# Performance work log

Hardware: AMD Instinct MI355X
Metric: run time of the kernel (lower is better)

## Reference

```python
import jax, jax.numpy as jnp
import numpy as np
import math

V, L, H, D, T_MAX, FF = 50257, 12, 12, 768, 1024, 3072
B, T = 2, 1024
HD = D // H


def layernorm(x, g, b, eps=1e-5):
    m = x.mean(-1, keepdims=True)
    v = ((x - m) ** 2).mean(-1, keepdims=True)
    return (x - m) / jnp.sqrt(v + eps) * g + b


def mgelu(x):
    # note: module uses 0.047715 (not the standard 0.044715)
    return 0.5 * x * (1.0 + jnp.tanh(math.sqrt(2.0 / math.pi) * (x + 0.047715 * x ** 3)))


def setup_inputs() -> dict:
    key = jax.random.key(0)
    ks = jax.random.split(key, 16)
    s = 0.02
    sr = 0.02 * (2 * L) ** -0.5  # residual-projection init per GPT2 paper
    inp = {
        "idx": jax.random.randint(ks[0], (B, T), 0, V),
        "targets": jax.random.randint(ks[1], (B, T), 0, V),
        "wte": jax.random.normal(ks[2], (V, D), jnp.float32) * s,
        "wpe": jax.random.normal(ks[3], (T_MAX, D), jnp.float32) * s,
        "ln1_g": jnp.ones((L, D), jnp.float32),
        "ln1_b": jnp.zeros((L, D), jnp.float32),
        "qkv_w": jax.random.normal(ks[4], (L, D, 3 * D), jnp.float32) * s,
        "qkv_b": jnp.zeros((L, 3 * D), jnp.float32),
        "po_w": jax.random.normal(ks[5], (L, D, D), jnp.float32) * sr,
        "po_b": jnp.zeros((L, D), jnp.float32),
        "ln2_g": jnp.ones((L, D), jnp.float32),
        "ln2_b": jnp.zeros((L, D), jnp.float32),
        "fc_w": jax.random.normal(ks[6], (L, D, FF), jnp.float32) * s,
        "fc_b": jnp.zeros((L, FF), jnp.float32),
        "pr_w": jax.random.normal(ks[7], (L, FF, D), jnp.float32) * sr,
        "pr_b": jnp.zeros((L, D), jnp.float32),
        "lnf_g": jnp.ones((D,), jnp.float32),
        "lnf_b": jnp.zeros((D,), jnp.float32),
        "lm_w": jax.random.normal(ks[8], (D, V), jnp.float32) * s,
    }
    return inp


def gpt_forward(idx, targets, wte, wpe, ln1_g, ln1_b, qkv_w, qkv_b, po_w, po_b,
                ln2_g, ln2_b, fc_w, fc_b, pr_w, pr_b, lnf_g, lnf_b, lm_w):
    Bt, Tt = idx.shape
    x = wte[idx] + wpe[:Tt]  # [B,T,D]
    causal = jnp.tril(jnp.ones((Tt, Tt), bool))
    scale = 1.0 / math.sqrt(HD)

    def block(x, p):
        g1, b1, wq, bq, wo, bo, g2, b2, wf, bf, wp, bp = p
        h = layernorm(x, g1, b1)
        qkv = h @ wq + bq  # [B,T,3D]
        q, k, v = jnp.split(qkv, 3, axis=-1)
        q = q.reshape(Bt, Tt, H, HD)
        k = k.reshape(Bt, Tt, H, HD)
        v = v.reshape(Bt, Tt, H, HD)
        att = jnp.einsum('bqhd,bkhd->bhqk', q, k) * scale
        att = jnp.where(causal, att, -jnp.inf)
        att = jax.nn.softmax(att, axis=-1)  # dropout = identity (eval)
        y = jnp.einsum('bhqk,bkhd->bqhd', att, v).reshape(Bt, Tt, D)
        x = x + y @ wo + bo
        h2 = layernorm(x, g2, b2)
        x = x + mgelu(h2 @ wf + bf) @ wp + bp
        return x, None

    x, _ = jax.lax.scan(block, x, (ln1_g, ln1_b, qkv_w, qkv_b, po_w, po_b,
                                   ln2_g, ln2_b, fc_w, fc_b, pr_w, pr_b))
    x = layernorm(x, lnf_g, lnf_b)
    logits = x @ lm_w  # [B,T,V]

    logp = jax.nn.log_softmax(logits, axis=-1)
    valid = targets >= 0  # ignore_index=-1
    tgt = jnp.where(valid, targets, 0)
    nll = -jnp.take_along_axis(logp, tgt[..., None], axis=-1)[..., 0]
    loss = (nll * valid).sum() / valid.sum()
    return logits, loss


def reference(idx, targets, wte, wpe, ln1_g, ln1_b, qkv_w, qkv_b, po_w, po_b,
              ln2_g, ln2_b, fc_w, fc_b, pr_w, pr_b, lnf_g, lnf_b, lm_w):
    return gpt_forward(idx, targets, wte, wpe, ln1_g, ln1_b, qkv_w, qkv_b, po_w, po_b,
                       ln2_g, ln2_b, fc_w, fc_b, pr_w, pr_b, lnf_g, lnf_b, lm_w)
```

## Files before the change

kernel.cpp:

```cpp
#include <hip/hip_runtime.h>
#include <hip/hip_bf16.h>
#include <math.h>

#define VOC 50257
#define NL 12
#define NH 12
#define DM 768
#define FF 3072
#define BB 2
#define TT 1024
#define MR (BB*TT)

typedef __attribute__((ext_vector_type(8))) short bf16x8;
typedef __attribute__((ext_vector_type(4))) float f32x4;

__device__ __forceinline__ float mgelu_f(float x) {
    return 0.5f*x*(1.f + tanhf(0.7978845608028654f*(x + 0.047715f*x*x*x)));
}

__device__ __forceinline__ unsigned short f2bf(float f) {
    __hip_bfloat16 h = __float2bfloat16(f);
    return *reinterpret_cast<unsigned short*>(&h);
}

#define GLDS(gptr, lptr) __builtin_amdgcn_global_load_lds( \
    (const __attribute__((address_space(1))) void*)(gptr), \
    (__attribute__((address_space(3))) void*)(lptr), 16, 0, 0)

__device__ __forceinline__ int xcd_work(int bid, int total) {
    int xcd = bid & 7;
    int seq = bid >> 3;
    int q = total >> 3, r = total & 7;
    int base = (xcd < r) ? xcd*(q+1) : r + xcd*q;
    return base + seq;
}

__global__ void embed_kernel(const int* __restrict__ idx, const float* __restrict__ wte,
                             const float* __restrict__ wpe, float* __restrict__ x) {
    int row = blockIdx.x;
    int t = row % TT;
    int tok = idx[row];
    for (int d = threadIdx.x; d < DM; d += blockDim.x)
        x[(size_t)row*DM + d] = wte[(size_t)tok*DM + d] + wpe[(size_t)t*DM + d];
}

__global__ __launch_bounds__(256) void ln_kernel(const float* __restrict__ x,
                          const float* __restrict__ g,
                          const float* __restrict__ b, __hip_bfloat16* __restrict__ out) {
    int row = blockIdx.x*4 + (threadIdx.x >> 6);
    int lane = threadIdx.x & 63;
    const float* xr = x + (size_t)row*DM;
    float vals[DM/64];
    float s = 0.f;
    #pragma unroll
    for (int i = 0; i < DM/64; i++) { vals[i] = xr[lane + i*64]; s += vals[i]; }
    #pragma unroll
    for (int off = 32; off > 0; off >>= 1) s += __shfl_xor(s, off);
    float mean = s * (1.0f/DM);
    float vs = 0.f;
    #pragma unroll
    for (int i = 0; i < DM/64; i++) { float d = vals[i]-mean; vs += d*d; }
    #pragma unroll
    for (int off = 32; off > 0; off >>= 1) vs += __shfl_xor(vs, off);
    float rstd = rsqrtf(vs * (1.0f/DM) + 1e-5f);
    #pragma unroll
    for (int i = 0; i < DM/64; i++) {
        int d = lane + i*64;
        out[(size_t)row*DM + d] = __float2bfloat16((vals[i]-mean)*rstd*g[d] + b[d]);
    }
}

struct TJob { const float* in; __hip_bfloat16* out; int R, C, cx, tile0; };

__device__ __forceinline__ void trans_one(const TJob& j, int t) {
    __shared__ float tile[32][33];
    int bx = t % j.cx, by = t / j.cx;
    int c0 = bx*32, r0 = by*32;
    int tx = threadIdx.x, ty = threadIdx.y;
    #pragma unroll
    for (int i = ty; i < 32; i += 8) {
        int r = r0 + i, c = c0 + tx;
        tile[i][tx] = (r < j.R && c < j.C) ? j.in[(size_t)r*j.C + c] : 0.f;
    }
    __syncthreads();
    #pragma unroll
    for (int i = ty; i < 32; i += 8) {
        int c = c0 + i, r = r0 + tx;
        if (c < j.C && r < j.R) j.out[(size_t)c*j.R + r] = __float2bfloat16(tile[tx][i]);
    }
}

__global__ void trans4_kernel(TJob j0, TJob j1, TJob j2, TJob j3) {
    int t = blockIdx.x;
    if (t >= j3.tile0)      trans_one(j3, t - j3.tile0);
    else if (t >= j2.tile0) trans_one(j2, t - j2.tile0);
    else if (t >= j1.tile0) trans_one(j1, t - j1.tile0);
    else                    trans_one(j0, t);
}

__global__ void trans1_kernel(TJob j0) { trans_one(j0, blockIdx.x); }

template<int MODE, int HALFM>
__global__ __launch_bounds__(256) void mfma_gemm_kernel(
        const __hip_bfloat16* __restrict__ A,
        const __hip_bfloat16* __restrict__ Wt,
        const float* __restrict__ bias,
        const float* __restrict__ res,
        void* __restrict__ Cout,
        __hip_bfloat16* __restrict__ vt,
        float* __restrict__ part,
        int M, int N, int K) {
    constexpr int BM = HALFM ? 64 : 128;
    constexpr int NF = HALFM ? 2 : 4;
    constexpr int ABM = BM*64;
    constexpr int SMEMB = 3*ABM + 3*8192;
    __shared__ __align__(16) char smem[SMEMB];
    char* As = smem;
    char* Bs = smem + 3*ABM;
    int tid = threadIdx.x;
    int lane = tid & 63, wid = tid >> 6;
    int kq = lane >> 4, lr = lane & 15;

    int nby = M / BM;
    int work = xcd_work(blockIdx.x, gridDim.x);
    int by = work % nby;
    int bx = work / nby;
    int m0 = by * BM, n0 = bx * 128;

    int wm = HALFM ? 0 : (wid >> 1);
    int wn = HALFM ? wid : (wid & 1);
    int colbase = HALFM ? wn*32 : wn*64;

    f32x4 acc[4][NF] = {};

    auto STAGE = [&](int slot, int k0) {
        if constexpr (HALFM) {
            GLDS(A + (size_t)(m0 + lane)*K + k0 + wid*8, As + slot*ABM + wid*1024);
            #pragma unroll
            for (int t = 0; t < 2; t++) {
                int lx = wid + t*4;
                int r  = (lx & 1)*64 + lane;
                int kk = (lx >> 1)*8;
                int nr = n0 + r; if (nr > N-1) nr = N-1;
                GLDS(Wt + (size_t)nr*K + k0 + kk, Bs + slot*8192 + lx*1024);
            }
        } else {
            #pragma unroll
            for (int t = 0; t < 2; t++) {
                int lx = wid + t*4;
                int r  = (lx & 1)*64 + lane;
                int kk = (lx >> 1)*8;
                GLDS(A + (size_t)(m0 + r)*K + k0 + kk, As + slot*ABM + lx*1024);
                int nr = n0 + r; if (nr > N-1) nr = N-1;
                GLDS(Wt + (size_t)nr*K + k0 + kk, Bs + slot*8192 + lx*1024);
            }
        }
    };

    int nk = K >> 5;
    STAGE(0, 0);
    STAGE(1, (1 < nk ? 1 : nk-1)*32);
    for (int ki = 0; ki < nk; ++ki) {
        int cur = ki % 3;
        int k2 = (ki+2 < nk ? ki+2 : nk-1)*32;
        STAGE((ki+2) % 3, k2);
        __builtin_amdgcn_sched_barrier(0);
        if constexpr (HALFM) asm volatile("s_waitcnt vmcnt(6)" ::: "memory");
        else                 asm volatile("s_waitcnt vmcnt(8)" ::: "memory");
        __builtin_amdgcn_s_barrier();
        __builtin_amdgcn_sched_barrier(0);

        bf16x8 afrag[4], bfrag[NF];
        #pragma unroll
        for (int m = 0; m < 4; m++)
            afrag[m] = *(const bf16x8*)(As + cur*ABM + kq*(BM*16) + (wm*64 + m*16 + lr)*16);
        #pragma unroll
        for (int n = 0; n < NF; n++)
            bfrag[n] = *(const bf16x8*)(Bs + cur*8192 + kq*2048 + (colbase + n*16 + lr)*16);
        #pragma unroll
        for (int m = 0; m < 4; m++)
            #pragma unroll
            for (int n = 0; n < NF; n++)
                acc[m][n] = __builtin_amdgcn_mfma_f32_16x16x32_bf16(afrag[m], bfrag[n], acc[m][n], 0, 0, 0);

        __builtin_amdgcn_sched_barrier(0);
        asm volatile("s_waitcnt lgkmcnt(0)" ::: "memory");
        __builtin_amdgcn_s_barrier();
    }

    if (MODE == 0) {
        float* eps = (float*)smem;
        int nbx = (N + 127) >> 7;
        int rl2 = tid >> 1, sub = tid & 1;
        float pm = -INFINITY, ps = 0.f;
        #pragma unroll
        for (int hh = 0; hh < 2; ++hh) {
            __syncthreads();
            if (wn == hh) {
                #pragma unroll
                for (int m = 0; m < 4; m++)
                    #pragma unroll
                    for (int n = 0; n < 4; n++) {
                        int cl = n*16 + lr;
                        #pragma unroll
                        for (int j = 0; j < 4; j++)
                            eps[(wm*64 + m*16 + kq*4 + j)*68 + cl] = acc[m][n][j];
                    }
            }
            __syncthreads();
            #pragma unroll
            for (int it = 0; it < 8; ++it) {
                int rl = it*16 + (tid >> 4);
                int c4 = tid & 15;
                int col = n0 + hh*64 + c4*4;
                int row = m0 + rl;
                f32x4 v = *(const f32x4*)(eps + rl*68 + c4*4);
                if (col + 3 < N) {
                    __builtin_nontemporal_store(v, (f32x4*)&((float*)Cout)[(size_t)row*N + col]);
                } else {
                    #pragma unroll
                    for (int u = 0; u < 4; ++u)
                        if (col + u < N)
                            __builtin_nontemporal_store(v[u], &((float*)Cout)[(size_t)row*N + col + u]);
                }
            }
            #pragma unroll
            for (int i = 0; i < 8; ++i) {
                f32x4 v = *(const f32x4*)(eps + rl2*68 + sub*32 + i*4);
                #pragma unroll
                for (int u = 0; u < 4; ++u) {
                    int col = n0 + hh*64 + sub*32 + i*4 + u;
                    float xv = (col < N) ? v[u] : -INFINITY;
                    if (xv > pm) { ps = ps*__expf(pm - xv); pm = xv; ps += 1.f; }
                    else ps += __expf(xv - pm);
                }
            }
        }
        float m2 = __shfl_xor(pm, 1), s2 = __shfl_xor(ps, 1);
        float Mx = fmaxf(pm, m2);
        float Sx = ps*__expf(pm - Mx) + s2*__expf(m2 - Mx);
        if (sub == 0)
            ((float2*)part)[(size_t)(m0 + rl2)*nbx + bx] = make_float2(Mx, Sx);
        return;
    }

    #pragma unroll
    for (int m = 0; m < 4; m++) {
        #pragma unroll
        for (int n = 0; n < NF; n++) {
            int col = n0 + colbase + n*16 + lr;
            if (col >= N) continue;
            float bv = bias[col];
            #pragma unroll
            for (int j = 0; j < 4; j++) {
                int row = m0 + wm*64 + m*16 + kq*4 + j;
                float v = acc[m][n][j] + bv;
                size_t o = (size_t)row*N + col;
                if (MODE == 1) {
                    __hip_bfloat16 bvv = __float2bfloat16(v);
                    ((__hip_bfloat16*)Cout)[o] = bvv;
                    if (col >= 2*DM) {
                        int hh = (col - 2*DM) >> 6, dd = (col - 2*DM) & 63;
                        int bb = row >> 10, tt = row & 1023;
                        vt[(((size_t)bb*NH + hh)*64 + dd)*TT + tt] = bvv;
                    }
                } else if (MODE == 2) {
                    ((float*)Cout)[o] = v + res[o];
                } else {
                    ((__hip_bfloat16*)Cout)[o] = __float2bfloat16(mgelu_f(v));
                }
            }
        }
    }
}

__global__ __launch_bounds__(256) void mfma_attn_kernel(const __hip_bfloat16* __restrict__ qkv,
                                                        const __hip_bfloat16* __restrict__ vt,
                                                        __hip_bfloat16* __restrict__ y) {
    __shared__ __align__(16) char K_lds[3][8192];
    __shared__ __align__(16) char VT_lds[3][8192];
    __shared__ __align__(16) char P_lds[4][2048];

    int work = xcd_work(blockIdx.x, BB*NH*16);
    int qt = 15 - (work & 15);
    int bh = work >> 4;
    int h  = bh % NH;
    int b  = bh / NH;
    int tid = threadIdx.x;
    int lane = tid & 63, w = tid >> 6;
    int lr = lane & 15, kq = lane >> 4;
    int q0 = qt * 64;

    int sr = lane >> 3;
    int scb = (lane & 7) * 16;

    int qrow = q0 + w*16 + lr;
    const __hip_bfloat16* qp = qkv + (size_t)(b*TT + qrow)*3*DM + h*64;
    bf16x8 qfrag[2];
    qfrag[0] = *(const bf16x8*)(qp + kq*8);
    qfrag[1] = *(const bf16x8*)(qp + 32 + kq*8);

    f32x4 oacc[4] = {};
    float m_run = -INFINITY, l_run = 0.f;
    const float scale = 0.125f;

    const char* kbase  = (const char*)qkv + ((size_t)b*TT*3*DM + DM + h*64)*2;
    const char* vtbase = (const char*)vt + ((size_t)(b*NH + h)*64)*TT*2;

    auto STAGE = [&](int slot, int kt) {
        int kv0 = kt*64;
        #pragma unroll
        for (int t = 0; t < 2; t++) {
            int lx = w + t*4;
            int r = lx*8 + sr;
            int cbs = scb ^ ((r & 7) << 4);
            GLDS(kbase + (size_t)(kv0 + r)*3*DM*2 + cbs, K_lds[slot] + lx*1024);
            GLDS(vtbase + (size_t)r*TT*2 + kv0*2 + cbs, VT_lds[slot] + lx*1024);
        }
    };

    STAGE(0, 0);
    STAGE(1, 1 <= qt ? 1 : qt);
    for (int kt = 0; kt <= qt; ++kt) {
        int cur = kt % 3;
        STAGE((kt+2) % 3, kt+2 <= qt ? kt+2 : qt);
        __builtin_amdgcn_sched_barrier(0);
        asm volatile("s_waitcnt vmcnt(8)" ::: "memory");
        __builtin_amdgcn_s_barrier();
        __builtin_amdgcn_sched_barrier(0);

        f32x4 st[4] = {};
        #pragma unroll
        for (int t = 0; t < 4; ++t) {
            #pragma unroll
            for (int ks = 0; ks < 2; ++ks) {
                int row = t*16 + lr;
                bf16x8 kf = *(const bf16x8*)(K_lds[cur] + row*128 + ((ks*64 + kq*16) ^ ((lr&7)<<4)));
                st[t] = __builtin_amdgcn_mfma_f32_16x16x32_bf16(kf, qfrag[ks], st[t], 0,0,0);
            }
        }

        float sv[4][4];
        bool diag = (kt == qt);
        float pmax = -INFINITY;
        #pragma unroll
        for (int t = 0; t < 4; ++t)
            #pragma unroll
            for (int jj = 0; jj < 4; ++jj) {
                float s = st[t][jj] * scale;
                if (diag && (t*16 + kq*4 + jj > w*16 + lr)) s = -INFINITY;
                sv[t][jj] = s;
                pmax = fmaxf(pmax, s);
            }
        pmax = fmaxf(pmax, __shfl_xor(pmax, 16));
        pmax = fmaxf(pmax, __shfl_xor(pmax, 32));
        float m_new = fmaxf(m_run, pmax);
        float corr = __expf(m_run - m_new);
        float rsum = 0.f;
        #pragma unroll
        for (int t = 0; t < 4; ++t)
            #pragma unroll
            for (int jj = 0; jj < 4; ++jj) {
                float p = __expf(sv[t][jj] - m_new);
                sv[t][jj] = p;
                rsum += p;
            }
        rsum += __shfl_xor(rsum, 16);
        rsum += __shfl_xor(rsum, 32);
        l_run = l_run * corr + rsum;
        m_run = m_new;

        #pragma unroll
        for (int jj = 0; jj < 4; ++jj) {
            float c = __shfl(corr, kq*20 + jj);
            #pragma unroll
            for (int nt = 0; nt < 4; ++nt) oacc[nt][jj] *= c;
        }

        #pragma unroll
        for (int t = 0; t < 4; ++t) {
            unsigned pk0 = (unsigned)f2bf(sv[t][0]) | ((unsigned)f2bf(sv[t][1]) << 16);
            unsigned pk1 = (unsigned)f2bf(sv[t][2]) | ((unsigned)f2bf(sv[t][3]) << 16);
            unsigned off = ((unsigned)(lr*128 + t*32 + kq*8)) ^ (((unsigned)lr&7u)<<4);
            *(uint2*)(P_lds[w] + off) = make_uint2(pk0, pk1);
        }

        #pragma unroll
        for (int ks = 0; ks < 2; ++ks) {
            bf16x8 pa = *(const bf16x8*)(P_lds[w] +
                ((unsigned)(lr*128 + ((ks*64 + kq*16) ^ ((lr&7)<<4)))));
            #pragma unroll
            for (int nt = 0; nt < 4; ++nt) {
                int row = nt*16 + lr;
                bf16x8 vf = *(const bf16x8*)(VT_lds[cur] + row*128 + ((ks*64 + kq*16) ^ ((lr&7)<<4)));
                oacc[nt] = __builtin_amdgcn_mfma_f32_16x16x32_bf16(pa, vf, oacc[nt], 0,0,0);
            }
        }

        __builtin_amdgcn_sched_barrier(0);
        asm volatile("s_waitcnt lgkmcnt(0)" ::: "memory");
        __builtin_amdgcn_s_barrier();
    }

    #pragma unroll
    for (int jj = 0; jj < 4; ++jj) {
        float li = __shfl(l_run, kq*20 + jj);
        int qg = q0 + w*16 + kq*4 + jj;
        #pragma unroll
        for (int nt = 0; nt < 4; ++nt)
            y[(size_t)(b*TT + qg)*DM + h*64 + nt*16 + lr] =
                __float2bfloat16(oacc[nt][jj] / li);
    }
}

__global__ void zero_acc_kernel(float* p) { p[threadIdx.x] = 0.f; }

__global__ __launch_bounds__(64) void loss_reduce_kernel(const float* __restrict__ part,
                                                         const float* __restrict__ logits,
                                                         const int* __restrict__ targets,
                                                         float* __restrict__ acc) {
    int row = blockIdx.x;
    int lane = threadIdx.x;
    const int nbx = (VOC + 127) >> 7;
    float m = -INFINITY, s = 0.f;
    for (int bx = lane; bx < nbx; bx += 64) {
        float2 p = ((const float2*)part)[(size_t)row*nbx + bx];
        float Mx = fmaxf(m, p.x);
        s = s*__expf(m - Mx) + p.y*__expf(p.x - Mx);
        m = Mx;
    }
    #pragma unroll
    for (int off = 32; off > 0; off >>= 1) {
        float m2 = __shfl_xor(m, off), s2 = __shfl_xor(s, off);
        float Mx = fmaxf(m, m2);
        s = s*__expf(m - Mx) + s2*__expf(m2 - Mx);
        m = Mx;
    }
    if (lane == 0) {
        int tgt = targets[row];
        if (tgt >= 0) {
            float lse = logf(s) + m;
            atomicAdd(&acc[0], lse - logits[(size_t)row*VOC + tgt]);
            atomicAdd(&acc[1], 1.f);
        }
    }
}

__global__ void loss_final_kernel(const float* acc, float* out) {
    out[0] = acc[0] / acc[1];
}

static inline TJob mkjob(const float* in, __hip_bfloat16* out, int R, int C, int tile0) {
    TJob j; j.in = in; j.out = out; j.R = R; j.C = C;
    j.cx = (C + 31)/32; j.tile0 = tile0;
    return j;
}

extern "C" void kernel_launch(void* const* d_in, const int* in_sizes, int n_in,
                              void* d_out, int out_size, void* d_ws, size_t ws_size,
                              hipStream_t stream) {
    const int*   idx     = (const int*)  d_in[0];
    const int*   targets = (const int*)  d_in[1];
    const float* wte     = (const float*)d_in[2];
    const float* wpe     = (const float*)d_in[3];
    const float* ln1_g   = (const float*)d_in[4];
    const float* ln1_b   = (const float*)d_in[5];
    const float* qkv_w   = (const float*)d_in[6];
    const float* qkv_b   = (const float*)d_in[7];
    const float* po_w    = (const float*)d_in[8];
    const float* po_b    = (const float*)d_in[9];
    const float* ln2_g   = (const float*)d_in[10];
    const float* ln2_b   = (const float*)d_in[11];
    const float* fc_w    = (const float*)d_in[12];
    const float* fc_b    = (const float*)d_in[13];
    const float* pr_w    = (const float*)d_in[14];
    const float* pr_b    = (const float*)d_in[15];
    const float* lnf_g   = (const float*)d_in[16];
    const float* lnf_b   = (const float*)d_in[17];
    const float* lm_w    = (const float*)d_in[18];

    float* logits = (float*)d_out;

    char* p = (char*)d_ws;
    float* x = (float*)p;                 p += (size_t)MR*DM*4;
    __hip_bfloat16* h    = (__hip_bfloat16*)p; p += (size_t)MR*DM*2;
    __hip_bfloat16* qkvb = (__hip_bfloat16*)p; p += (size_t)MR*3*DM*2;
    __hip_bfloat16* yb   = (__hip_bfloat16*)p; p += (size_t)MR*DM*2;
    __hip_bfloat16* fb   = (__hip_bfloat16*)p; p += (size_t)MR*FF*2;
    __hip_bfloat16* vtb  = (__hip_bfloat16*)p; p += (size_t)BB*NH*64*TT*2;
    __hip_bfloat16* lm_wt  = (__hip_bfloat16*)p; p += (size_t)VOC*DM*2;
    __hip_bfloat16* qkv_wt = (__hip_bfloat16*)p; p += (size_t)3*DM*DM*2;
    __hip_bfloat16* po_wt  = (__hip_bfloat16*)p; p += (size_t)DM*DM*2;
    __hip_bfloat16* fc_wt  = (__hip_bfloat16*)p; p += (size_t)FF*DM*2;
    __hip_bfloat16* pr_wt  = (__hip_bfloat16*)p; p += (size_t)DM*FF*2;
    float* part = (float*)p;              p += (size_t)MR*((VOC+127)/128)*2*4;
    float* lacc = (float*)p;

    dim3 tpb(32, 8);

    embed_kernel<<<MR, 256, 0, stream>>>(idx, wte, wpe, x);

    {
        TJob j = mkjob(lm_w, lm_wt, DM, VOC, 0);
        int tiles = j.cx * ((DM+31)/32);
        trans1_kernel<<<tiles, tpb, 0, stream>>>(j);
    }

    for (int l = 0; l < NL; l++) {
        TJob j0 = mkjob(qkv_w + (size_t)l*DM*3*DM, qkv_wt, DM, 3*DM, 0);
        int t1 = j0.cx * 24;
        TJob j1 = mkjob(po_w + (size_t)l*DM*DM, po_wt, DM, DM, t1);
        int t2 = t1 + j1.cx * 24;
        TJob j2 = mkjob(fc_w + (size_t)l*DM*FF, fc_wt, DM, FF, t2);
        int t3 = t2 + j2.cx * 24;
        TJob j3 = mkjob(pr_w + (size_t)l*FF*DM, pr_wt, FF, DM, t3);
        int tot = t3 + j3.cx * 96;
        trans4_kernel<<<tot, tpb, 0, stream>>>(j0, j1, j2, j3);

        ln_kernel<<<MR/4, 256, 0, stream>>>(x, ln1_g + l*DM, ln1_b + l*DM, h);
        mfma_gemm_kernel<1,0><<<(3*DM/128)*(MR/128), 256, 0, stream>>>(
            h, qkv_wt, qkv_b + (size_t)l*3*DM, nullptr, qkvb, vtb, nullptr, MR, 3*DM, DM);
        mfma_attn_kernel<<<BB*NH*(TT/64), 256, 0, stream>>>(qkvb, vtb, yb);
        mfma_gemm_kernel<2,1><<<(DM/128)*(MR/64), 256, 0, stream>>>(
            yb, po_wt, po_b + (size_t)l*DM, x, x, nullptr, nullptr, MR, DM, DM);
        ln_kernel<<<MR/4, 256, 0, stream>>>(x, ln2_g + l*DM, ln2_b + l*DM, h);
        mfma_gemm_kernel<3,0><<<(FF/128)*(MR/128), 256, 0, stream>>>(
            h, fc_wt, fc_b + (size_t)l*FF, nullptr, fb, nullptr, nullptr, MR, FF, DM);
        mfma_gemm_kernel<2,1><<<(DM/128)*(MR/64), 256, 0, stream>>>(
            fb, pr_wt, pr_b + (size_t)l*DM, x, x, nullptr, nullptr, MR, DM, FF);
    }

    ln_kernel<<<MR/4, 256, 0, stream>>>(x, lnf_g, lnf_b, h);
    mfma_gemm_kernel<0,0><<<((VOC+127)/128)*(MR/128), 256, 0, stream>>>(
        h, lm_wt, nullptr, nullptr, logits, nullptr, part, MR, VOC, DM);

    zero_acc_kernel<<<1, 2, 0, stream>>>(lacc);
    loss_reduce_kernel<<<MR, 64, 0, stream>>>(part, logits, targets, lacc);
    loss_final_kernel<<<1, 1, 0, stream>>>(lacc, logits + (size_t)MR*VOC);
}
```

Measured before the change: 2.868 ms.

## Batch all weight transposes into one launch, add MFMA priority, two-pass softmax partials

All per-layer weight transposes and the LM-head transpose now run in a single kernel writing into per-layer buffers, and that kernel also zeroes the loss accumulator. This removes 12 separate transpose launches plus the zero kernel, and the larger grid fills the device better, at the cost of more workspace memory. MFMA sections in the GEMM and attention kernels are wrapped in s_setprio so matrix work is issued ahead of other waves. The LM-head epilogue switches from an online per-element max/rescale to a two-pass max-then-sum, which removes branches and repeated exponent rescaling.

```diff
diff --git a/kernel.cpp b/kernel.cpp
--- a/kernel.cpp
+++ b/kernel.cpp
@@ -70,35 +70,58 @@
     }
 }
 
-struct TJob { const float* in; __hip_bfloat16* out; int R, C, cx, tile0; };
-
-__device__ __forceinline__ void trans_one(const TJob& j, int t) {
-    __shared__ float tile[32][33];
-    int bx = t % j.cx, by = t / j.cx;
+#define TPL_QKV 1728
+#define TPL_PO   576
+#define TPL_FC  2304
+#define TPL_PR  2304
+#define TPL_LAYER (TPL_QKV + TPL_PO + TPL_FC + TPL_PR)
+#define TPL_LM  37704
+#define TPL_TOTAL (NL*TPL_LAYER + TPL_LM)
+
+__device__ __forceinline__ void trans_one(float (*tile)[33],
+                                          const float* __restrict__ in,
+                                          __hip_bfloat16* __restrict__ out,
+                                          int R, int C, int cx, int t) {
+    int bx = t % cx, by = t / cx;
     int c0 = bx*32, r0 = by*32;
     int tx = threadIdx.x, ty = threadIdx.y;
     #pragma unroll
     for (int i = ty; i < 32; i += 8) {
         int r = r0 + i, c = c0 + tx;
-        tile[i][tx] = (r < j.R && c < j.C) ? j.in[(size_t)r*j.C + c] : 0.f;
+        tile[i][tx] = (r < R && c < C) ? in[(size_t)r*C + c] : 0.f;
     }
     __syncthreads();
     #pragma unroll
     for (int i = ty; i < 32; i += 8) {
         int c = c0 + i, r = r0 + tx;
-        if (c < j.C && r < j.R) j.out[(size_t)c*j.R + r] = __float2bfloat16(tile[tx][i]);
-    }
-}
-
-__global__ void trans4_kernel(TJob j0, TJob j1, TJob j2, TJob j3) {
-    int t = blockIdx.x;
-    if (t >= j3.tile0)      trans_one(j3, t - j3.tile0);
-    else if (t >= j2.tile0) trans_one(j2, t - j2.tile0);
-    else if (t >= j1.tile0) trans_one(j1, t - j1.tile0);
-    else                    trans_one(j0, t);
-}
-
-__global__ void trans1_kernel(TJob j0) { trans_one(j0, blockIdx.x); }
+        if (c < C && r < R) out[(size_t)c*R + r] = __float2bfloat16(tile[tx][i]);
+    }
+}
+
+__global__ void trans_all_kernel(const float* __restrict__ qkv_w, const float* __restrict__ po_w,
+                                 const float* __restrict__ fc_w, const float* __restrict__ pr_w,
+                                 const float* __restrict__ lm_w,
+                                 __hip_bfloat16* qkv_wt, __hip_bfloat16* po_wt,
+                                 __hip_bfloat16* fc_wt, __hip_bfloat16* pr_wt,
+                                 __hip_bfloat16* lm_wt, float* lacc) {
+    __shared__ float tile[32][33];
+    int bid = blockIdx.x;
+    if (bid == 0 && threadIdx.y == 0 && threadIdx.x < 2) lacc[threadIdx.x] = 0.f;
+    if (bid < NL*TPL_LAYER) {
+        int l = bid / TPL_LAYER;
+        int r = bid - l*TPL_LAYER;
+        if (r < TPL_QKV)
+            trans_one(tile, qkv_w + (size_t)l*DM*3*DM, qkv_wt + (size_t)l*3*DM*DM, DM, 3*DM, 72, r);
+        else if (r < TPL_QKV + TPL_PO)
+            trans_one(tile, po_w + (size_t)l*DM*DM, po_wt + (size_t)l*DM*DM, DM, DM, 24, r - TPL_QKV);
+        else if (r < TPL_QKV + TPL_PO + TPL_FC)
+            trans_one(tile, fc_w + (size_t)l*DM*FF, fc_wt + (size_t)l*DM*FF, DM, FF, 96, r - TPL_QKV - TPL_PO);
+        else
+            trans_one(tile, pr_w + (size_t)l*FF*DM, pr_wt + (size_t)l*FF*DM, FF, DM, 24, r - TPL_QKV - TPL_PO - TPL_FC);
+    } else {
+        trans_one(tile, lm_w, lm_wt, DM, VOC, 1571, bid - NL*TPL_LAYER);
+    }
+}
 
 template<int MODE, int HALFM>
 __global__ __launch_bounds__(256) void mfma_gemm_kernel(
@@ -177,11 +200,13 @@
         #pragma unroll
         for (int n = 0; n < NF; n++)
             bfrag[n] = *(const bf16x8*)(Bs + cur*8192 + kq*2048 + (colbase + n*16 + lr)*16);
+        __builtin_amdgcn_s_setprio(1);
         #pragma unroll
         for (int m = 0; m < 4; m++)
             #pragma unroll
             for (int n = 0; n < NF; n++)
                 acc[m][n] = __builtin_amdgcn_mfma_f32_16x16x32_bf16(afrag[m], bfrag[n], acc[m][n], 0, 0, 0);
+        __builtin_amdgcn_s_setprio(0);
 
         __builtin_amdgcn_sched_barrier(0);
         asm volatile("s_waitcnt lgkmcnt(0)" ::: "memory");
@@ -224,15 +249,26 @@
                             __builtin_nontemporal_store(v[u], &((float*)Cout)[(size_t)row*N + col + u]);
                 }
             }
+            float hm = -INFINITY;
             #pragma unroll
             for (int i = 0; i < 8; ++i) {
                 f32x4 v = *(const f32x4*)(eps + rl2*68 + sub*32 + i*4);
                 #pragma unroll
                 for (int u = 0; u < 4; ++u) {
                     int col = n0 + hh*64 + sub*32 + i*4 + u;
-                    float xv = (col < N) ? v[u] : -INFINITY;
-                    if (xv > pm) { ps = ps*__expf(pm - xv); pm = xv; ps += 1.f; }
-                    else ps += __expf(xv - pm);
+                    hm = fmaxf(hm, (col < N) ? v[u] : -INFINITY);
+                }
+            }
+            float nm = fmaxf(pm, hm);
+            ps *= __expf(pm - nm);
+            pm = nm;
+            #pragma unroll
+            for (int i = 0; i < 8; ++i) {
+                f32x4 v = *(const f32x4*)(eps + rl2*68 + sub*32 + i*4);
+                #pragma unroll
+                for (int u = 0; u < 4; ++u) {
+                    int col = n0 + hh*64 + sub*32 + i*4 + u;
+                    ps += __expf(((col < N) ? v[u] : -INFINITY) - pm);
                 }
             }
         }
@@ -330,6 +366,7 @@
         __builtin_amdgcn_sched_barrier(0);
 
         f32x4 st[4] = {};
+        __builtin_amdgcn_s_setprio(1);
         #pragma unroll
         for (int t = 0; t < 4; ++t) {
             #pragma unroll
@@ -339,6 +376,7 @@
                 st[t] = __builtin_amdgcn_mfma_f32_16x16x32_bf16(kf, qfrag[ks], st[t], 0,0,0);
             }
         }
+        __builtin_amdgcn_s_setprio(0);
 
         float sv[4][4];
         bool diag = (kt == qt);
@@ -385,6 +423,7 @@
             *(uint2*)(P_lds[w] + off) = make_uint2(pk0, pk1);
         }
 
+        __builtin_amdgcn_s_setprio(1);
         #pragma unroll
         for (int ks = 0; ks < 2; ++ks) {
             bf16x8 pa = *(const bf16x8*)(P_lds[w] +
@@ -396,6 +435,7 @@
                 oacc[nt] = __builtin_amdgcn_mfma_f32_16x16x32_bf16(pa, vf, oacc[nt], 0,0,0);
             }
         }
+        __builtin_amdgcn_s_setprio(0);
 
         __builtin_amdgcn_sched_barrier(0);
         asm volatile("s_waitcnt lgkmcnt(0)" ::: "memory");
@@ -412,8 +452,6 @@
                 __float2bfloat16(oacc[nt][jj] / li);
     }
 }
-
-__global__ void zero_acc_kernel(float* p) { p[threadIdx.x] = 0.f; }
 
 __global__ __launch_bounds__(64) void loss_reduce_kernel(const float* __restrict__ part,
                                                          const float* __restrict__ logits,
@@ -448,12 +486,6 @@
 
 __global__ void loss_final_kernel(const float* acc, float* out) {
     out[0] = acc[0] / acc[1];
-}
-
-static inline TJob mkjob(const float* in, __hip_bfloat16* out, int R, int C, int tile0) {
-    TJob j; j.in = in; j.out = out; j.R = R; j.C = C;
-    j.cx = (C + 31)/32; j.tile0 = tile0;
-    return j;
 }
 
 extern "C" void kernel_launch(void* const* d_in, const int* in_sizes, int n_in,
@@ -489,52 +521,36 @@
     __hip_bfloat16* fb   = (__hip_bfloat16*)p; p += (size_t)MR*FF*2;
     __hip_bfloat16* vtb  = (__hip_bfloat16*)p; p += (size_t)BB*NH*64*TT*2;
     __hip_bfloat16* lm_wt  = (__hip_bfloat16*)p; p += (size_t)VOC*DM*2;
-    __hip_bfloat16* qkv_wt = (__hip_bfloat16*)p; p += (size_t)3*DM*DM*2;
-    __hip_bfloat16* po_wt  = (__hip_bfloat16*)p; p += (size_t)DM*DM*2;
-    __hip_bfloat16* fc_wt  = (__hip_bfloat16*)p; p += (size_t)FF*DM*2;
-    __hip_bfloat16* pr_wt  = (__hip_bfloat16*)p; p += (size_t)DM*FF*2;
+    __hip_bfloat16* qkv_wt = (__hip_bfloat16*)p; p += (size_t)NL*3*DM*DM*2;
+    __hip_bfloat16* po_wt  = (__hip_bfloat16*)p; p += (size_t)NL*DM*DM*2;
+    __hip_bfloat16* fc_wt  = (__hip_bfloat16*)p; p += (size_t)NL*DM*FF*2;
+    __hip_bfloat16* pr_wt  = (__hip_bfloat16*)p; p += (size_t)NL*DM*FF*2;
     float* part = (float*)p;              p += (size_t)MR*((VOC+127)/128)*2*4;
     float* lacc = (float*)p;
 
-    dim3 tpb(32, 8);
-
     embed_kernel<<<MR, 256, 0, stream>>>(idx, wte, wpe, x);
 
-    {
-        TJob j = mkjob(lm_w, lm_wt, DM, VOC, 0);
-        int tiles = j.cx * ((DM+31)/32);
-        trans1_kernel<<<tiles, tpb, 0, stream>>>(j);
-    }
+    trans_all_kernel<<<TPL_TOTAL, dim3(32, 8), 0, stream>>>(
+        qkv_w, po_w, fc_w, pr_w, lm_w, qkv_wt, po_wt, fc_wt, pr_wt, lm_wt, lacc);
 
     for (int l = 0; l < NL; l++) {
-        TJob j0 = mkjob(qkv_w + (size_t)l*DM*3*DM, qkv_wt, DM, 3*DM, 0);
-        int t1 = j0.cx * 24;
-        TJob j1 = mkjob(po_w + (size_t)l*DM*DM, po_wt, DM, DM, t1);
-        int t2 = t1 + j1.cx * 24;
-        TJob j2 = mkjob(fc_w + (size_t)l*DM*FF, fc_wt, DM, FF, t2);
-        int t3 = t2 + j2.cx * 24;
-        TJob j3 = mkjob(pr_w + (size_t)l*FF*DM, pr_wt, FF, DM, t3);
-        int tot = t3 + j3.cx * 96;
-        trans4_kernel<<<tot, tpb, 0, stream>>>(j0, j1, j2, j3);
-
         ln_kernel<<<MR/4, 256, 0, stream>>>(x, ln1_g + l*DM, ln1_b + l*DM, h);
         mfma_gemm_kernel<1,0><<<(3*DM/128)*(MR/128), 256, 0, stream>>>(
-            h, qkv_wt, qkv_b + (size_t)l*3*DM, nullptr, qkvb, vtb, nullptr, MR, 3*DM, DM);
+            h, qkv_wt + (size_t)l*3*DM*DM, qkv_b + (size_t)l*3*DM, nullptr, qkvb, vtb, nullptr, MR, 3*DM, DM);
         mfma_attn_kernel<<<BB*NH*(TT/64), 256, 0, stream>>>(qkvb, vtb, yb);
         mfma_gemm_kernel<2,1><<<(DM/128)*(MR/64), 256, 0, stream>>>(
-            yb, po_wt, po_b + (size_t)l*DM, x, x, nullptr, nullptr, MR, DM, DM);
+            yb, po_wt + (size_t)l*DM*DM, po_b + (size_t)l*DM, x, x, nullptr, nullptr, MR, DM, DM);
         ln_kernel<<<MR/4, 256, 0, stream>>>(x, ln2_g + l*DM, ln2_b + l*DM, h);
         mfma_gemm_kernel<3,0><<<(FF/128)*(MR/128), 256, 0, stream>>>(
-            h, fc_wt, fc_b + (size_t)l*FF, nullptr, fb, nullptr, nullptr, MR, FF, DM);
+            h, fc_wt + (size_t)l*DM*FF, fc_b + (size_t)l*FF, nullptr, fb, nullptr, nullptr, MR, FF, DM);
         mfma_gemm_kernel<2,1><<<(DM/128)*(MR/64), 256, 0, stream>>>(
-            fb, pr_wt, pr_b + (size_t)l*DM, x, x, nullptr, nullptr, MR, DM, FF);
+            fb, pr_wt + (size_t)l*DM*FF, pr_b + (size_t)l*DM, x, x, nullptr, nullptr, MR, DM, FF);
     }
 
     ln_kernel<<<MR/4, 256, 0, stream>>>(x, lnf_g, lnf_b, h);
     mfma_gemm_kernel<0,0><<<((VOC+127)/128)*(MR/128), 256, 0, stream>>>(
         h, lm_wt, nullptr, nullptr, logits, nullptr, part, MR, VOC, DM);
 
-    zero_acc_kernel<<<1, 2, 0, stream>>>(lacc);
     loss_reduce_kernel<<<MR, 64, 0, stream>>>(part, logits, targets, lacc);
     loss_final_kernel<<<1, 1, 0, stream>>>(lacc, logits + (size_t)MR*VOC);
 }
```

After: 2.995 ms. 1.04x slower.
